# Optimization experiments

Hardware: AMD Instinct MI355X
Metric: run time of the kernel (lower is better)

Reference implementation:

```python
import jax, jax.numpy as jnp
import numpy as np

B, N, M, C = 8, 8192, 2048, 256
EPS = 1e-8


def setup_inputs() -> dict:
    key = jax.random.key(0)
    k1, k2, k3 = jax.random.split(key, 3)
    unknown = jax.random.uniform(k1, (B, N, 3), dtype=jnp.float32)
    known = jax.random.uniform(k2, (B, M, 3), dtype=jnp.float32)
    known_feats = jax.random.normal(k3, (B, C, M), dtype=jnp.float32)
    return {"unknown": unknown, "known": known, "known_feats": known_feats}


def reference(unknown, known, known_feats):
    # three_nn: brute-force squared distances (B, n, m); pointnet2's CUDA
    # three_nn returns SQUARED distances, matching 1/(d2 + eps) weighting.
    diff = unknown[:, :, None, :] - known[:, None, :, :]  # (B, n, m, 3)
    d2 = jnp.sum(diff * diff, axis=-1)                    # (B, n, m)
    neg_d2, idx = jax.lax.top_k(-d2, 3)                   # 3 smallest distances
    dist = -neg_d2                                        # (B, n, 3)
    dist_recip = 1.0 / (dist + EPS)
    weight = dist_recip / jnp.sum(dist_recip, axis=2, keepdims=True)  # (B, n, 3)
    # three_interpolate: gather the 3 neighbor features and weighted-sum.
    feats_t = jnp.swapaxes(known_feats, 1, 2)             # (B, m, C)
    gathered = jax.vmap(lambda f, i: f[i])(feats_t, idx)  # (B, n, 3, C)
    new_features = jnp.einsum("bnkc,bnk->bcn", gathered, weight)  # (B, C, n)
    return new_features
```

## Files before the change

### kernel.cpp

```cpp
#include <hip/hip_runtime.h>


#define BB 8
#define NN 8192
#define MM 2048
#define CC 256
#define EPSV 1e-8f
#define PTS 128
#define NTH 512
#define NCH 8
#define CHUNK (MM/NCH)

#define INS(dd, mi, D0,I0,D1,I1,D2,I2) \
    if ((dd) < D2) { \
        if ((dd) < D1) { D2 = D1; I2 = I1; \
            if ((dd) < D0) { D1 = D0; I1 = I0; D0 = (dd); I0 = (mi); } \
            else           { D1 = (dd); I1 = (mi); } \
        } else { D2 = (dd); I2 = (mi); } }

#define PINS(dd, mi, D0,I0,D1,I1,D2,I2) { \
    const bool c0 = (dd) < D0, c1 = (dd) < D1, c2 = (dd) < D2; \
    I2 = c1 ? I1 : (c2 ? (mi) : I2); \
    I1 = c0 ? I0 : (c1 ? (mi) : I1); \
    I0 = c0 ? (mi) : I0; \
    D2 = __builtin_amdgcn_fmed3f(D1, D2, (dd)); \
    D1 = __builtin_amdgcn_fmed3f(D0, D1, (dd)); \
    D0 = fminf(D0, (dd)); }

#define STEP(KX,KY,KZ,MI) { \
    { const float dx = uxA-(KX), dy = uyA-(KY), dz = uzA-(KZ); \
      const float d = __fadd_rn(__fadd_rn(__fmul_rn(dx,dx),__fmul_rn(dy,dy)),__fmul_rn(dz,dz)); \
      PINS(d, MI, dA0,iA0,dA1,iA1,dA2,iA2) } \
    { const float dx = uxB-(KX), dy = uyB-(KY), dz = uzB-(KZ); \
      const float d = __fadd_rn(__fadd_rn(__fmul_rn(dx,dx),__fmul_rn(dy,dy)),__fmul_rn(dz,dz)); \
      PINS(d, MI, dB0,iB0,dB1,iB1,dB2,iB2) } }

__global__ __launch_bounds__(NTH) void fp_interp_kernel(
    const float* __restrict__ unknown,
    const float* __restrict__ known,
    const float* __restrict__ feats,
    float* __restrict__ out)
{
    __shared__ float kxs[MM];
    __shared__ float kys[MM];
    __shared__ float kzs[MM];
    __shared__ float pd[NCH][PTS][3];
    __shared__ int   pi[NCH][PTS][3];
    __shared__ float sw[3][PTS];
    __shared__ int   si[3][PTS];

    const int tilesPerBatch = NN / PTS;
    const int b    = blockIdx.x / tilesPerBatch;
    const int tile = blockIdx.x % tilesPerBatch;
    const int t    = threadIdx.x;
    const int p    = t & 63;
    const int g    = t >> 6;

    const float* kb = known + (size_t)b * MM * 3;
    for (int idx = t; idx < MM * 3; idx += NTH) {
        const float v  = kb[idx];
        const int   a  = idx % 3;
        const int   mi = idx / 3;
        float* dst = (a == 0) ? kxs : ((a == 1) ? kys : kzs);
        dst[mi] = v;
    }
    __syncthreads();

    const float* uA = unknown + ((size_t)b * NN + (size_t)tile * PTS + p) * 3;
    const float uxA = uA[0], uyA = uA[1], uzA = uA[2];
    const float* uB = uA + 64 * 3;
    const float uxB = uB[0], uyB = uB[1], uzB = uB[2];

    float dA0=1e30f, dA1=1e30f, dA2=1e30f; int iA0=0, iA1=0, iA2=0;
    float dB0=1e30f, dB1=1e30f, dB2=1e30f; int iB0=0, iB1=0, iB2=0;

    const int mbeg = g * CHUNK;
    #pragma unroll 2
    for (int m = mbeg; m < mbeg + CHUNK; m += 4) {
        const float4 x4 = *reinterpret_cast<const float4*>(&kxs[m]);
        const float4 y4 = *reinterpret_cast<const float4*>(&kys[m]);
        const float4 z4 = *reinterpret_cast<const float4*>(&kzs[m]);
        STEP(x4.x, y4.x, z4.x, m)
        STEP(x4.y, y4.y, z4.y, m+1)
        STEP(x4.z, y4.z, z4.z, m+2)
        STEP(x4.w, y4.w, z4.w, m+3)
    }

    pd[g][p][0] = dA0; pd[g][p][1] = dA1; pd[g][p][2] = dA2;
    pi[g][p][0] = iA0; pi[g][p][1] = iA1; pi[g][p][2] = iA2;
    pd[g][p+64][0] = dB0; pd[g][p+64][1] = dB1; pd[g][p+64][2] = dB2;
    pi[g][p+64][0] = iB0; pi[g][p+64][1] = iB1; pi[g][p+64][2] = iB2;
    __syncthreads();

    if (t < PTS) {
        float e0=1e30f, e1=1e30f, e2=1e30f; int j0=0, j1=0, j2=0;
        #pragma unroll
        for (int q = 0; q < NCH; ++q) {
            #pragma unroll
            for (int r = 0; r < 3; ++r) {
                const float d  = pd[q][t][r];
                const int   ii = pi[q][t][r];
                INS(d, ii, e0,j0,e1,j1,e2,j2)
            }
        }
        const float r0 = 1.0f / (e0 + EPSV);
        const float r1 = 1.0f / (e1 + EPSV);
        const float r2 = 1.0f / (e2 + EPSV);
        const float rs = r0 + r1 + r2;
        sw[0][t] = r0 / rs; sw[1][t] = r1 / rs; sw[2][t] = r2 / rs;
        si[0][t] = j0;      si[1][t] = j1;      si[2][t] = j2;
    }
    __syncthreads();

    const int pp = t & 127;
    const int cg = t >> 7;
    const float w0 = sw[0][pp], w1 = sw[1][pp], w2 = sw[2][pp];
    const int   j0 = si[0][pp], j1 = si[1][pp], j2 = si[2][pp];
    const float* fb = feats + (size_t)b * CC * MM;
    float* ob = out + (size_t)b * CC * NN + (size_t)tile * PTS;

    #pragma unroll 4
    for (int c = cg; c < CC; c += 4) {
        const float* fr = fb + (size_t)c * MM;
        ob[(size_t)c * NN + pp] = w0 * fr[j0] + w1 * fr[j1] + w2 * fr[j2];
    }
}

extern "C" void kernel_launch(void* const* d_in, const int* in_sizes, int n_in,
                              void* d_out, int out_size, void* d_ws, size_t ws_size,
                              hipStream_t stream) {
    const float* unknown = (const float*)d_in[0];
    const float* known   = (const float*)d_in[1];
    const float* feats   = (const float*)d_in[2];
    float* out = (float*)d_out;

    const int nBlocks = BB * (NN / PTS);
    fp_interp_kernel<<<nBlocks, NTH, 0, stream>>>(unknown, known, feats, out);
}
```

Measured before the change: 183.5 us.

## Split NN scan and interpolation into two kernels with LDS-staged feature rows

Splits the fused kernel into a nearest-neighbor scan kernel that writes weights and indices to workspace, and a separate interpolation kernel. The interpolation kernel stages 4 feature channels (4×2048 floats) per block in LDS and gathers from there, so there are no scattered global reads of feature rows. In exchange it adds a second launch and a workspace round trip for weights and indices, which every channel-tile block re-reads. The interpolation grid is only 512 blocks, each with a 32 KB LDS buffer.

```diff
diff --git a/kernel.cpp b/kernel.cpp
--- a/kernel.cpp
+++ b/kernel.cpp
@@ -10,6 +10,7 @@
 #define NTH 512
 #define NCH 8
 #define CHUNK (MM/NCH)
+#define TC 4
 
 #define INS(dd, mi, D0,I0,D1,I1,D2,I2) \
     if ((dd) < D2) { \
@@ -35,19 +36,17 @@
       const float d = __fadd_rn(__fadd_rn(__fmul_rn(dx,dx),__fmul_rn(dy,dy)),__fmul_rn(dz,dz)); \
       PINS(d, MI, dB0,iB0,dB1,iB1,dB2,iB2) } }
 
-__global__ __launch_bounds__(NTH) void fp_interp_kernel(
+__global__ __launch_bounds__(NTH) void nn_scan_kernel(
     const float* __restrict__ unknown,
     const float* __restrict__ known,
-    const float* __restrict__ feats,
-    float* __restrict__ out)
+    float4* __restrict__ wgt4,
+    int4*  __restrict__ idx4)
 {
     __shared__ float kxs[MM];
     __shared__ float kys[MM];
     __shared__ float kzs[MM];
     __shared__ float pd[NCH][PTS][3];
     __shared__ int   pi[NCH][PTS][3];
-    __shared__ float sw[3][PTS];
-    __shared__ int   si[3][PTS];
 
     const int tilesPerBatch = NN / PTS;
     const int b    = blockIdx.x / tilesPerBatch;
@@ -107,22 +106,43 @@
         const float r1 = 1.0f / (e1 + EPSV);
         const float r2 = 1.0f / (e2 + EPSV);
         const float rs = r0 + r1 + r2;
-        sw[0][t] = r0 / rs; sw[1][t] = r1 / rs; sw[2][t] = r2 / rs;
-        si[0][t] = j0;      si[1][t] = j1;      si[2][t] = j2;
+        const int gp = b * NN + tile * PTS + t;
+        wgt4[gp] = make_float4(r0 / rs, r1 / rs, r2 / rs, 0.0f);
+        idx4[gp] = make_int4(j0, j1, j2, 0);
     }
+}
+
+__global__ __launch_bounds__(NTH) void interp_kernel(
+    const float* __restrict__ feats,
+    const float4* __restrict__ wgt4,
+    const int4*  __restrict__ idx4,
+    float* __restrict__ out)
+{
+    __shared__ float fbuf[TC * MM];
+
+    const int tilesPerB = CC / TC;
+    const int b  = blockIdx.x / tilesPerB;
+    const int c0 = (blockIdx.x % tilesPerB) * TC;
+    const int t  = threadIdx.x;
+
+    const float4* src = reinterpret_cast<const float4*>(
+        feats + ((size_t)b * CC + c0) * MM);
+    #pragma unroll
+    for (int i = t; i < TC * MM / 4; i += NTH)
+        reinterpret_cast<float4*>(fbuf)[i] = src[i];
     __syncthreads();
 
-    const int pp = t & 127;
-    const int cg = t >> 7;
-    const float w0 = sw[0][pp], w1 = sw[1][pp], w2 = sw[2][pp];
-    const int   j0 = si[0][pp], j1 = si[1][pp], j2 = si[2][pp];
-    const float* fb = feats + (size_t)b * CC * MM;
-    float* ob = out + (size_t)b * CC * NN + (size_t)tile * PTS;
-
-    #pragma unroll 4
-    for (int c = cg; c < CC; c += 4) {
-        const float* fr = fb + (size_t)c * MM;
-        ob[(size_t)c * NN + pp] = w0 * fr[j0] + w1 * fr[j1] + w2 * fr[j2];
+    #pragma unroll 2
+    for (int it = 0; it < NN / NTH; ++it) {
+        const int n = it * NTH + t;
+        const float4 w = wgt4[b * NN + n];
+        const int4   j = idx4[b * NN + n];
+        float* ob = out + ((size_t)b * CC + c0) * NN + n;
+        #pragma unroll
+        for (int cl = 0; cl < TC; ++cl) {
+            const float* fr = fbuf + cl * MM;
+            ob[(size_t)cl * NN] = w.x * fr[j.x] + w.y * fr[j.y] + w.z * fr[j.z];
+        }
     }
 }
 
@@ -134,6 +154,9 @@
     const float* feats   = (const float*)d_in[2];
     float* out = (float*)d_out;
 
-    const int nBlocks = BB * (NN / PTS);
-    fp_interp_kernel<<<nBlocks, NTH, 0, stream>>>(unknown, known, feats, out);
+    float4* wgt4 = (float4*)d_ws;
+    int4*   idx4 = (int4*)((char*)d_ws + (size_t)BB * NN * sizeof(float4));
+
+    nn_scan_kernel<<<BB * (NN / PTS), NTH, 0, stream>>>(unknown, known, wgt4, idx4);
+    interp_kernel<<<BB * (CC / TC), NTH, 0, stream>>>(feats, wgt4, idx4, out);
 }
```

Result: faster. 151.8 us (-17.3%).
